# Kernel tuning notes

Hardware: AMD Instinct MI355X
Metric: run time of the kernel (lower is better)

The kernel has to match this reference:

```python
import jax, jax.numpy as jnp
import numpy as np

B, S, H = 2, 2048, 1024
E, K, F = 8, 2, 4096


def setup_inputs() -> dict:
    key = jax.random.key(0)
    ks = jax.random.split(key, 7)
    s_h = 1.0 / np.sqrt(H)
    s_f = 1.0 / np.sqrt(F)
    return {
        "hidden_states": jax.random.normal(ks[0], (B, S, H), jnp.float32),
        "Wr": jax.random.normal(ks[1], (H, E), jnp.float32) * s_h,
        "br": jnp.zeros((E,), jnp.float32),
        "W1": jax.random.normal(ks[2], (E, H, F), jnp.float32) * s_h,
        "b1": jnp.zeros((E, F), jnp.float32),
        "W2": jax.random.normal(ks[3], (E, F, H), jnp.float32) * s_f,
        "b2": jnp.zeros((E, H), jnp.float32),
    }


def _moe_forward(hidden_states, Wr, br, W1, b1, W2, b2):
    b, s, h = hidden_states.shape
    x = hidden_states.reshape(-1, h)  # [T, H]
    # --- router: top-k over softmax probs, renormalized ---
    logits = x @ Wr + br  # [T, E]
    probs = jax.nn.softmax(logits, axis=-1)
    top_w, top_i = jax.lax.top_k(probs, K)  # [T, K]
    weights = top_w / jnp.sum(top_w, axis=-1, keepdims=True)  # [T, K]
    # --- dense-equivalent expert dispatch + combine ---
    # per-token per-expert combine weight (zero for unselected experts)
    out = jnp.zeros_like(x)
    for e in range(E):
        w_e = jnp.sum(weights * (top_i == e), axis=-1)  # [T]
        h_e = jax.nn.gelu(x @ W1[e] + b1[e], approximate=False)  # [T, F]
        y_e = h_e @ W2[e] + b2[e]  # [T, H]
        out = out + w_e[:, None] * y_e
    # --- aux load-balance loss (counts are constants wrt grads) ---
    counts = jnp.sum(jax.nn.one_hot(top_i, E, dtype=logits.dtype), axis=(0, 1))  # [E]
    load = counts / (top_i.size)
    aux_loss = jnp.mean((load - 1.0 / E) ** 2)
    # --- z-loss ---
    z_loss = jnp.mean(jax.nn.logsumexp(logits, axis=-1))
    total_loss = 0.01 * aux_loss + 0.001 * z_loss
    return out.reshape(b, s, h), total_loss


def reference(hidden_states, Wr, br, W1, b1, W2, b2):
    output, total_loss = _moe_forward(hidden_states, Wr, br, W1, b1, W2, b2)
    return output, total_loss
```

## Files before the change

### kernel.cpp

```cpp
#include <hip/hip_runtime.h>
#include <stdint.h>
#include <math.h>

#define T_TOK 4096
#define H_DIM 1024
#define E_EXP 8
#define F_DIM 4096
#define NASSIGN (T_TOK * 2)
#define OUT_ELEMS ((size_t)T_TOK * H_DIM)
#define YB_ELEMS ((size_t)8192 * H_DIM)

typedef unsigned short u16;
typedef __attribute__((ext_vector_type(8))) short short8;
typedef __attribute__((ext_vector_type(4))) short short4v;
typedef __attribute__((ext_vector_type(4))) float f32x4;

__device__ __forceinline__ u16 f2bf(float f) {
  union { float f; uint32_t u; } c; c.f = f;
  uint32_t u = c.u;
  return (u16)((u + 0x7FFFu + ((u >> 16) & 1u)) >> 16);
}

__device__ __forceinline__ float fast_erf(float u) {
  const float au = fabsf(u);
  const float t = __builtin_amdgcn_rcpf(__builtin_fmaf(0.3275911f, au, 1.0f));
  float p = __builtin_fmaf(1.061405429f, t, -1.453152027f);
  p = __builtin_fmaf(p, t, 1.421413741f);
  p = __builtin_fmaf(p, t, -0.284496736f);
  p = __builtin_fmaf(p, t, 0.254829592f);
  p = p * t;
  const float y = __builtin_fmaf(-p, __expf(-au * au), 1.0f);
  return copysignf(y, u);
}

__device__ __forceinline__ void gl_lds16(const void* g, void* l) {
  __builtin_amdgcn_global_load_lds(
      (const __attribute__((address_space(1))) uint32_t*)g,
      (__attribute__((address_space(3))) uint32_t*)(uintptr_t)l, 16, 0, 0);
}


__device__ __forceinline__ void transpose_tile(
    const float* __restrict__ in, u16* __restrict__ out, int R, int C,
    int bx, int by, int bz, u16 (*tile)[72]) {
  const size_t eoff = (size_t)bz * R * C;
  {
    const int c4 = (threadIdx.x & 15) * 4;
    const int rr = threadIdx.x >> 4;
    const float* inp = in + eoff + ((size_t)by * 64) * C + bx * 64;
#pragma unroll
    for (int p = 0; p < 4; ++p) {
      const int r = rr + p * 16;
      const float4 v = *(const float4*)(inp + (size_t)r * C + c4);
      tile[r][c4 + 0] = f2bf(v.x); tile[r][c4 + 1] = f2bf(v.y);
      tile[r][c4 + 2] = f2bf(v.z); tile[r][c4 + 3] = f2bf(v.w);
    }
  }
  __syncthreads();
  {
    u16* op = out + (((size_t)bz * (C >> 6) + bx) * (R >> 6) + by) * 4096;
#pragma unroll
    for (int p = 0; p < 2; ++p) {
      const int c = (threadIdx.x >> 3) + p * 32;
      const int rg = (threadIdx.x & 7) * 8;
      short8 o;
#pragma unroll
      for (int j = 0; j < 8; ++j) o[j] = (short)tile[rg + j][c];
      *(short8*)(op + c * 64 + rg) = o;
    }
  }
}

__global__ __launch_bounds__(256) void prep_kernel(
    const float* __restrict__ x, const float* __restrict__ Wr,
    const float* __restrict__ br, u16* __restrict__ xb,
    int* __restrict__ tki, float* __restrict__ tkw,
    int* __restrict__ counts, float* __restrict__ zsum,
    const float* __restrict__ W1, u16* __restrict__ w1t,
    const float* __restrict__ W2, u16* __restrict__ w2t) {
  __shared__ u16 tile[64][72];
  __shared__ int lcnt[8];
  __shared__ float lzv[16];
  const int id = blockIdx.x;

  if (id >= 256) {
    if (id < 8448) {
      const int q = id - 256;
      transpose_tile(W1, w1t, H_DIM, F_DIM, q & 63, (q >> 6) & 15, q >> 10, tile);
    } else {
      const int q = id - 8448;
      transpose_tile(W2, w2t, F_DIM, H_DIM, q & 15, (q >> 4) & 63, q >> 10, tile);
    }
    return;
  }

  const int wave = threadIdx.x >> 6;
  const int lane = threadIdx.x & 63;
  if (threadIdx.x < 8) lcnt[threadIdx.x] = 0;
  __syncthreads();
#pragma unroll
  for (int it = 0; it < 4; ++it) {
    const int t = id * 16 + wave * 4 + it;
    const float* xr = x + (size_t)t * H_DIM;
    u16* xbr = xb + (size_t)t * H_DIM;
    float acc[8];
#pragma unroll
    for (int e = 0; e < 8; ++e) acc[e] = 0.0f;
#pragma unroll
    for (int j = 0; j < 4; ++j) {
      const int h0 = j * 256 + lane * 4;
      const float4 xv = *(const float4*)(xr + h0);
      const float vv[4] = {xv.x, xv.y, xv.z, xv.w};
      short4v pk;
#pragma unroll
      for (int i = 0; i < 4; ++i) {
        pk[i] = (short)f2bf(vv[i]);
        const float4 w0 = *(const float4*)(Wr + (size_t)(h0 + i) * 8);
        const float4 w1 = *(const float4*)(Wr + (size_t)(h0 + i) * 8 + 4);
        acc[0] += vv[i] * w0.x; acc[1] += vv[i] * w0.y;
        acc[2] += vv[i] * w0.z; acc[3] += vv[i] * w0.w;
        acc[4] += vv[i] * w1.x; acc[5] += vv[i] * w1.y;
        acc[6] += vv[i] * w1.z; acc[7] += vv[i] * w1.w;
      }
      *(short4v*)(xbr + h0) = pk;
    }
#pragma unroll
    for (int e = 0; e < 8; ++e) {
      float v = acc[e];
#pragma unroll
      for (int s = 32; s > 0; s >>= 1) v += __shfl_xor(v, s);
      acc[e] = v;
    }
    if (lane == 0) {
      float l[8];
#pragma unroll
      for (int e = 0; e < 8; ++e) l[e] = acc[e] + br[e];
      float mx = l[0];
#pragma unroll
      for (int e = 1; e < 8; ++e) mx = fmaxf(mx, l[e]);
      float p[8], s = 0.0f;
#pragma unroll
      for (int e = 0; e < 8; ++e) { p[e] = __expf(l[e] - mx); s += p[e]; }
      int i0 = 0;
#pragma unroll
      for (int e = 1; e < 8; ++e) if (p[e] > p[i0]) i0 = e;
      int i1 = (i0 == 0) ? 1 : 0;
#pragma unroll
      for (int e = 0; e < 8; ++e) if (e != i1 && e != i0 && p[e] > p[i1]) i1 = e;
      const float ws = p[i0] + p[i1];
      tki[2 * t] = i0; tki[2 * t + 1] = i1;
      tkw[2 * t] = p[i0] / ws; tkw[2 * t + 1] = p[i1] / ws;
      atomicAdd(&lcnt[i0], 1);
      atomicAdd(&lcnt[i1], 1);
      lzv[wave * 4 + it] = mx + logf(s);
    }
  }
  __syncthreads();
  if (threadIdx.x < 8) {
    const int c = lcnt[threadIdx.x];
    if (c) atomicAdd(&counts[threadIdx.x], c);
  }
  if (threadIdx.x == 64) {
    float zs = 0.0f;
#pragma unroll
    for (int i = 0; i < 16; ++i) zs += lzv[i];
    atomicAdd(zsum, zs);
  }
}

__global__ void scatter_kernel(const int* __restrict__ tki, const float* __restrict__ tkw,
                               const int* __restrict__ counts, int* __restrict__ cursor,
                               int* __restrict__ perm, float* __restrict__ pw,
                               int* __restrict__ islot,
                               const float* __restrict__ zsum, float* __restrict__ out_loss) {
  int offs[8];
  {
    int a = 0;
#pragma unroll
    for (int e = 0; e < 8; ++e) { offs[e] = a; a += counts[e]; }
  }
  const int lane = threadIdx.x & 63;
  const int t = blockIdx.x * 256 + threadIdx.x;
#pragma unroll
  for (int k = 0; k < 2; ++k) {
    const int e = tki[2 * t + k];
    int slot = 0;
#pragma unroll
    for (int ee = 0; ee < 8; ++ee) {
      const unsigned long long mask = __ballot(e == ee);
      if (mask) {
        const int leader = __ffsll(mask) - 1;
        int b = 0;
        if (lane == leader) b = atomicAdd(&cursor[ee], (int)__popcll(mask));
        b = __shfl(b, leader);
        if (e == ee) {
          const int r = (int)__popcll(mask & ((1ull << lane) - 1ull));
          slot = offs[ee] + b + r;
        }
      }
    }
    perm[slot] = t;
    pw[slot] = tkw[2 * t + k];
    islot[2 * t + k] = slot;
  }
  if (blockIdx.x == 0 && threadIdx.x == 0) {
    float aux = 0.0f;
#pragma unroll
    for (int e = 0; e < 8; ++e) {
      const float d = (float)counts[e] / (float)NASSIGN - 0.125f;
      aux += d * d;
    }
    aux *= (1.0f / 8.0f);
    out_loss[0] = 0.01f * aux + 0.001f * (zsum[0] / (float)T_TOK);
  }
}


__global__ __launch_bounds__(256, 4) void gemm1_kernel(
    const u16* __restrict__ xb, const u16* __restrict__ w1t,
    const float* __restrict__ b1, const int* __restrict__ perm,
    const int* __restrict__ cnts, u16* __restrict__ hbuf) {
  const int id = blockIdx.x;
  const int e = id & 7;
  const int wq = id >> 3;
  const int n0 = (wq & 31) << 7;
  const int m0 = (wq >> 5) << 7;
  int cnt, off;
  {
    int a = 0, c = 0;
#pragma unroll
    for (int i = 0; i < 8; ++i) { const int ci = cnts[i]; if (i < e) a += ci; if (i == e) c = ci; }
    cnt = c; off = a;
  }
  if (m0 >= cnt) return;

  __shared__ __align__(16) u16 smem[16384];
  u16* As = smem;
  u16* Bs = smem + 8192;

  const int tid = threadIdx.x;
  const int rbase = tid >> 3;
  const int kc = ((tid & 7) ^ (rbase & 7)) * 8;

  const u16* ap[4];
#pragma unroll
  for (int l = 0; l < 4; ++l) {
    int ra = m0 + rbase + l * 32; if (ra > cnt - 1) ra = cnt - 1;
    ap[l] = xb + (size_t)perm[off + ra] * H_DIM + kc;
  }
  const u16* bp0 = w1t + ((((size_t)e * (F_DIM >> 6) + (n0 >> 6)) * (H_DIM >> 6)) << 12)
                 + rbase * 64 + kc;
  const size_t bnt = (size_t)(H_DIM >> 6) << 12;

  const int wave = tid >> 6, lane = tid & 63;
  const int wm = (wave >> 1) * 64, wn = (wave & 1) * 64;
  const int lr = lane & 15, q = lane >> 4;
  const int qs0 = q ^ (lr & 7), qs1 = (4 + q) ^ (lr & 7);

  f32x4 acc[4][4];
#pragma unroll
  for (int i = 0; i < 4; ++i)
#pragma unroll
    for (int j = 0; j < 4; ++j) acc[i][j] = (f32x4)0.0f;

  const short8* Afr = (const short8*)As;
  const short8* Bfr = (const short8*)Bs;

  for (int k0 = 0; k0 < (H_DIM >> 6); ++k0) {
    gl_lds16(ap[0], &As[(size_t)tid * 8]);
    gl_lds16(ap[1], &As[(size_t)(tid + 256) * 8]);
    gl_lds16(ap[2], &As[(size_t)(tid + 512) * 8]);
    gl_lds16(ap[3], &As[(size_t)(tid + 768) * 8]);
    gl_lds16(bp0,              &Bs[(size_t)tid * 8]);
    gl_lds16(bp0 + 2048,       &Bs[(size_t)(tid + 256) * 8]);
    gl_lds16(bp0 + bnt,        &Bs[(size_t)(tid + 512) * 8]);
    gl_lds16(bp0 + bnt + 2048, &Bs[(size_t)(tid + 768) * 8]);
#pragma unroll
    for (int l = 0; l < 4; ++l) ap[l] += 64;
    bp0 += 4096;
    __syncthreads();
#pragma unroll
    for (int s = 0; s < 2; ++s) {
      const int qs = s ? qs1 : qs0;
      short8 a[4], b[4];
#pragma unroll
      for (int i = 0; i < 4; ++i) a[i] = Afr[(wm + i * 16 + lr) * 8 + qs];
#pragma unroll
      for (int j = 0; j < 4; ++j) b[j] = Bfr[(wn + j * 16 + lr) * 8 + qs];
#pragma unroll
      for (int i = 0; i < 4; ++i)
#pragma unroll
        for (int j = 0; j < 4; ++j)
          acc[i][j] = __builtin_amdgcn_mfma_f32_16x16x32_bf16(a[i], b[j], acc[i][j], 0, 0, 0);
    }
    __syncthreads();
  }

#pragma unroll
  for (int i = 0; i < 4; ++i) {
#pragma unroll
    for (int rr = 0; rr < 4; ++rr) {
      const int row = wm + i * 16 + q * 4 + rr;
#pragma unroll
      for (int j = 0; j < 4; ++j) {
        const int col = wn + j * 16 + lr;
        const float v = acc[i][j][rr] + b1[e * F_DIM + n0 + col];
        const float g = 0.5f * v * (1.0f + fast_erf(v * 0.70710678118654752f));
        smem[(row << 7) + (col ^ (q << 4))] = f2bf(g);
      }
    }
  }
  __syncthreads();
#pragma unroll
  for (int p = 0; p < 8; ++p) {
    const int ml = p * 16 + (tid >> 4);
    const int nl = (tid & 15) * 8;
    const int m = m0 + ml;
    if (m < cnt) {
      const int qq = (ml >> 2) & 3;
      *(short8*)(hbuf + (size_t)(off + m) * F_DIM + n0 + nl) =
          *(const short8*)(smem + (ml << 7) + (nl ^ (qq << 4)));
    }
  }
}

__global__ __launch_bounds__(256, 4) void gemm2_kernel(
    const u16* __restrict__ hbuf, const u16* __restrict__ w2t,
    const float* __restrict__ b2, const float* __restrict__ pw,
    const int* __restrict__ cnts, float* __restrict__ ybuf) {
  const int id = blockIdx.x;
  const int e = id & 7;
  const int wq = id >> 3;
  const int n0 = (wq & 7) << 7;
  const int ks = (wq >> 3) & 1;
  const int m0 = (wq >> 4) << 7;
  int cnt, off;
  {
    int a = 0, c = 0;
#pragma unroll
    for (int i = 0; i < 8; ++i) { const int ci = cnts[i]; if (i < e) a += ci; if (i == e) c = ci; }
    cnt = c; off = a;
  }
  if (m0 >= cnt) return;

  __shared__ __align__(16) u16 As[128 * 64];
  __shared__ __align__(16) u16 Bs[128 * 64];

  const int tid = threadIdx.x;
  const int rbase = tid >> 3;
  const int kc = ((tid & 7) ^ (rbase & 7)) * 8;

  const u16* ap[4];
#pragma unroll
  for (int l = 0; l < 4; ++l) {
    int ra = m0 + rbase + l * 32; if (ra > cnt - 1) ra = cnt - 1;
    ap[l] = hbuf + (size_t)(off + ra) * F_DIM + (ks << 11) + kc;
  }
  const u16* bp0 = w2t + ((((size_t)e * (H_DIM >> 6) + (n0 >> 6)) * (F_DIM >> 6)) << 12)
                 + ((size_t)(ks << 5) << 12) + rbase * 64 + kc;
  const size_t bnt = (size_t)(F_DIM >> 6) << 12;

  const int wave = tid >> 6, lane = tid & 63;
  const int wm = (wave >> 1) * 64, wn = (wave & 1) * 64;
  const int lr = lane & 15, q = lane >> 4;
  const int qs0 = q ^ (lr & 7), qs1 = (4 + q) ^ (lr & 7);

  f32x4 acc[4][4];
#pragma unroll
  for (int i = 0; i < 4; ++i)
#pragma unroll
    for (int j = 0; j < 4; ++j) acc[i][j] = (f32x4)0.0f;

  const short8* Afr = (const short8*)As;
  const short8* Bfr = (const short8*)Bs;

  for (int k0 = 0; k0 < 32; ++k0) {
    gl_lds16(ap[0], &As[(size_t)tid * 8]);
    gl_lds16(ap[1], &As[(size_t)(tid + 256) * 8]);
    gl_lds16(ap[2], &As[(size_t)(tid + 512) * 8]);
    gl_lds16(ap[3], &As[(size_t)(tid + 768) * 8]);
    gl_lds16(bp0,              &Bs[(size_t)tid * 8]);
    gl_lds16(bp0 + 2048,       &Bs[(size_t)(tid + 256) * 8]);
    gl_lds16(bp0 + bnt,        &Bs[(size_t)(tid + 512) * 8]);
    gl_lds16(bp0 + bnt + 2048, &Bs[(size_t)(tid + 768) * 8]);
#pragma unroll
    for (int l = 0; l < 4; ++l) ap[l] += 64;
    bp0 += 4096;
    __syncthreads();
#pragma unroll
    for (int s = 0; s < 2; ++s) {
      const int qs = s ? qs1 : qs0;
      short8 a[4], b[4];
#pragma unroll
      for (int i = 0; i < 4; ++i) a[i] = Afr[(wm + i * 16 + lr) * 8 + qs];
#pragma unroll
      for (int j = 0; j < 4; ++j) b[j] = Bfr[(wn + j * 16 + lr) * 8 + qs];
#pragma unroll
      for (int i = 0; i < 4; ++i)
#pragma unroll
        for (int j = 0; j < 4; ++j)
          acc[i][j] = __builtin_amdgcn_mfma_f32_16x16x32_bf16(a[i], b[j], acc[i][j], 0, 0, 0);
    }
    __syncthreads();
  }

  float* yb = ybuf + (size_t)ks * YB_ELEMS;
#pragma unroll
  for (int i = 0; i < 4; ++i) {
#pragma unroll
    for (int rr = 0; rr < 4; ++rr) {
      const int m = m0 + wm + i * 16 + q * 4 + rr;
      if (m < cnt) {
        const int slot = off + m;
        const float w = pw[slot];
        float* orow = yb + (size_t)slot * H_DIM;
#pragma unroll
        for (int j = 0; j < 4; ++j) {
          const int col = n0 + wn + j * 16 + lr;
          float y = acc[i][j][rr];
          if (ks == 0) y += b2[e * H_DIM + col];
          orow[col] = w * y;
        }
      }
    }
  }
}

__global__ __launch_bounds__(256) void combine_kernel(
    const float* __restrict__ ybuf, const int* __restrict__ islot,
    float* __restrict__ out) {
  const int t = blockIdx.x;
  const int s0 = islot[2 * t];
  const int s1 = islot[2 * t + 1];
  const int c = threadIdx.x * 4;
  const float4 a0 = *(const float4*)(ybuf + (size_t)s0 * H_DIM + c);
  const float4 a1 = *(const float4*)(ybuf + YB_ELEMS + (size_t)s0 * H_DIM + c);
  const float4 b0 = *(const float4*)(ybuf + (size_t)s1 * H_DIM + c);
  const float4 b1 = *(const float4*)(ybuf + YB_ELEMS + (size_t)s1 * H_DIM + c);
  float4 r;
  r.x = a0.x + a1.x + b0.x + b1.x;
  r.y = a0.y + a1.y + b0.y + b1.y;
  r.z = a0.z + a1.z + b0.z + b1.z;
  r.w = a0.w + a1.w + b0.w + b1.w;
  *(float4*)(out + (size_t)t * H_DIM + c) = r;
}


extern "C" void kernel_launch(void* const* d_in, const int* in_sizes, int n_in,
                              void* d_out, int out_size, void* d_ws, size_t ws_size,
                              hipStream_t stream) {
  const float* x  = (const float*)d_in[0];
  const float* Wr = (const float*)d_in[1];
  const float* br = (const float*)d_in[2];
  const float* W1 = (const float*)d_in[3];
  const float* b1 = (const float*)d_in[4];
  const float* W2 = (const float*)d_in[5];
  const float* b2 = (const float*)d_in[6];
  float* out = (float*)d_out;

  char* ws = (char*)d_ws;
  u16* xb    = (u16*)(ws);
  u16* w1t   = (u16*)(ws + 8388608ull);
  u16* w2t   = (u16*)(ws + 75497472ull);
  u16* hbuf  = (u16*)(ws + 142606336ull);
  float* ybuf = (float*)(ws + 8388608ull);
  int*   tki    = (int*)(ws + 209715200ull);
  float* tkw    = (float*)(ws + 209747968ull);
  int*   perm   = (int*)(ws + 209780736ull);
  float* pw     = (float*)(ws + 209813504ull);
  int*   counts = (int*)(ws + 209846272ull);
  int*   cursor = counts + 8;
  float* zsum   = (float*)(counts + 16);
  int*   islot  = (int*)(ws + 209846400ull);

  hipMemsetAsync(counts, 0, 128, stream);

  prep_kernel<<<16640, 256, 0, stream>>>(x, Wr, br, xb, tki, tkw, counts, zsum,
                                         W1, w1t, W2, w2t);
  scatter_kernel<<<T_TOK / 256, 256, 0, stream>>>(tki, tkw, counts, cursor, perm, pw,
                                                  islot, zsum, out + OUT_ELEMS);
  gemm1_kernel<<<8192, 256, 0, stream>>>(xb, w1t, b1, perm, counts, hbuf);
  gemm2_kernel<<<4096, 256, 0, stream>>>(hbuf, w2t, b2, pw, counts, ybuf);
  combine_kernel<<<T_TOK, 256, 0, stream>>>(ybuf, islot, out);
}
```

Baseline: 608.9 us.

## Enlarge expert GEMM tiles to 256x256 with double-buffered LDS staging

Both expert GEMM kernels move from 128x128 to 256x256 output tiles per workgroup, with each wave computing a 128x128 sub-tile from an 8x8 accumulator array. LDS is double-buffered (two 64 KB stages) and the next K-slice is issued before computing the current one, with an explicit vmcnt wait and raw barriers. The aim is more reuse per loaded byte and overlap of global loads with MFMA work. In exchange, occupancy drops to one workgroup per CU with heavy register pressure, and there are fewer blocks to cover ragged per-expert token counts. The transpose tile padding also changes from 72 to 73.

```diff
diff --git a/kernel.cpp b/kernel.cpp
--- a/kernel.cpp
+++ b/kernel.cpp
@@ -39,10 +39,15 @@
       (__attribute__((address_space(3))) uint32_t*)(uintptr_t)l, 16, 0, 0);
 }
 
+__device__ __forceinline__ void wg_barrier() {
+  asm volatile("" ::: "memory");
+  __builtin_amdgcn_s_barrier();
+  asm volatile("" ::: "memory");
+}
 
 __device__ __forceinline__ void transpose_tile(
     const float* __restrict__ in, u16* __restrict__ out, int R, int C,
-    int bx, int by, int bz, u16 (*tile)[72]) {
+    int bx, int by, int bz, u16 (*tile)[73]) {
   const size_t eoff = (size_t)bz * R * C;
   {
     const int c4 = (threadIdx.x & 15) * 4;
@@ -78,7 +83,7 @@
     int* __restrict__ counts, float* __restrict__ zsum,
     const float* __restrict__ W1, u16* __restrict__ w1t,
     const float* __restrict__ W2, u16* __restrict__ w2t) {
-  __shared__ u16 tile[64][72];
+  __shared__ u16 tile[64][73];
   __shared__ int lcnt[8];
   __shared__ float lzv[16];
   const int id = blockIdx.x;
@@ -216,15 +221,45 @@
 }
 
 
-__global__ __launch_bounds__(256, 4) void gemm1_kernel(
+#define STAGE16(BUFOFF)                                                  \
+  {                                                                      \
+    const int nb_ = (BUFOFF);                                            \
+    _Pragma("unroll")                                                    \
+    for (int l = 0; l < 8; ++l) {                                        \
+      gl_lds16(ap[l], &smem[nb_ + l * 2048 + tid * 8]);          ap[l] += 64; \
+      gl_lds16(bp[l], &smem[nb_ + 16384 + l * 2048 + tid * 8]);  bp[l] += 4096; \
+    }                                                                    \
+  }
+
+#define COMPUTE256(BUFOFF)                                               \
+  {                                                                      \
+    const short8* Af = (const short8*)(smem + (BUFOFF));                 \
+    const short8* Bf = Af + 2048;                                        \
+    _Pragma("unroll")                                                    \
+    for (int s = 0; s < 2; ++s) {                                        \
+      const int qs = s ? qs1 : qs0;                                      \
+      short8 a[8];                                                       \
+      _Pragma("unroll")                                                  \
+      for (int i = 0; i < 8; ++i) a[i] = Af[(wm + i * 16 + lr) * 8 + qs]; \
+      _Pragma("unroll")                                                  \
+      for (int j = 0; j < 8; ++j) {                                      \
+        const short8 b = Bf[(wn + j * 16 + lr) * 8 + qs];                \
+        _Pragma("unroll")                                                \
+        for (int i = 0; i < 8; ++i)                                      \
+          acc[i][j] = __builtin_amdgcn_mfma_f32_16x16x32_bf16(a[i], b, acc[i][j], 0, 0, 0); \
+      }                                                                  \
+    }                                                                    \
+  }
+
+__global__ __launch_bounds__(256, 1) void gemm1_kernel(
     const u16* __restrict__ xb, const u16* __restrict__ w1t,
     const float* __restrict__ b1, const int* __restrict__ perm,
     const int* __restrict__ cnts, u16* __restrict__ hbuf) {
   const int id = blockIdx.x;
   const int e = id & 7;
   const int wq = id >> 3;
-  const int n0 = (wq & 31) << 7;
-  const int m0 = (wq >> 5) << 7;
+  const int n0 = (wq & 15) << 8;
+  const int m0 = (wq >> 4) << 8;
   int cnt, off;
   {
     int a = 0, c = 0;
@@ -234,106 +269,90 @@
   }
   if (m0 >= cnt) return;
 
-  __shared__ __align__(16) u16 smem[16384];
-  u16* As = smem;
-  u16* Bs = smem + 8192;
+  __shared__ __align__(16) u16 smem[65536];
 
   const int tid = threadIdx.x;
   const int rbase = tid >> 3;
   const int kc = ((tid & 7) ^ (rbase & 7)) * 8;
 
-  const u16* ap[4];
-#pragma unroll
-  for (int l = 0; l < 4; ++l) {
+  const u16* ap[8];
+#pragma unroll
+  for (int l = 0; l < 8; ++l) {
     int ra = m0 + rbase + l * 32; if (ra > cnt - 1) ra = cnt - 1;
     ap[l] = xb + (size_t)perm[off + ra] * H_DIM + kc;
   }
-  const u16* bp0 = w1t + ((((size_t)e * (F_DIM >> 6) + (n0 >> 6)) * (H_DIM >> 6)) << 12)
-                 + rbase * 64 + kc;
-  const size_t bnt = (size_t)(H_DIM >> 6) << 12;
+  const u16* bp[8];
+#pragma unroll
+  for (int l = 0; l < 8; ++l)
+    bp[l] = w1t + (((size_t)e * (F_DIM >> 6) + (n0 >> 6) + (l >> 1)) * (H_DIM >> 6)) * 4096
+          + ((l & 1) * 32 + rbase) * 64 + kc;
 
   const int wave = tid >> 6, lane = tid & 63;
-  const int wm = (wave >> 1) * 64, wn = (wave & 1) * 64;
+  const int wm = (wave >> 1) * 128, wn = (wave & 1) * 128;
   const int lr = lane & 15, q = lane >> 4;
   const int qs0 = q ^ (lr & 7), qs1 = (4 + q) ^ (lr & 7);
 
-  f32x4 acc[4][4];
-#pragma unroll
-  for (int i = 0; i < 4; ++i)
-#pragma unroll
-    for (int j = 0; j < 4; ++j) acc[i][j] = (f32x4)0.0f;
-
-  const short8* Afr = (const short8*)As;
-  const short8* Bfr = (const short8*)Bs;
-
-  for (int k0 = 0; k0 < (H_DIM >> 6); ++k0) {
-    gl_lds16(ap[0], &As[(size_t)tid * 8]);
-    gl_lds16(ap[1], &As[(size_t)(tid + 256) * 8]);
-    gl_lds16(ap[2], &As[(size_t)(tid + 512) * 8]);
-    gl_lds16(ap[3], &As[(size_t)(tid + 768) * 8]);
-    gl_lds16(bp0,              &Bs[(size_t)tid * 8]);
-    gl_lds16(bp0 + 2048,       &Bs[(size_t)(tid + 256) * 8]);
-    gl_lds16(bp0 + bnt,        &Bs[(size_t)(tid + 512) * 8]);
-    gl_lds16(bp0 + bnt + 2048, &Bs[(size_t)(tid + 768) * 8]);
-#pragma unroll
-    for (int l = 0; l < 4; ++l) ap[l] += 64;
-    bp0 += 4096;
-    __syncthreads();
-#pragma unroll
-    for (int s = 0; s < 2; ++s) {
-      const int qs = s ? qs1 : qs0;
-      short8 a[4], b[4];
-#pragma unroll
-      for (int i = 0; i < 4; ++i) a[i] = Afr[(wm + i * 16 + lr) * 8 + qs];
-#pragma unroll
-      for (int j = 0; j < 4; ++j) b[j] = Bfr[(wn + j * 16 + lr) * 8 + qs];
-#pragma unroll
-      for (int i = 0; i < 4; ++i)
-#pragma unroll
-        for (int j = 0; j < 4; ++j)
-          acc[i][j] = __builtin_amdgcn_mfma_f32_16x16x32_bf16(a[i], b[j], acc[i][j], 0, 0, 0);
-    }
-    __syncthreads();
-  }
-
-#pragma unroll
-  for (int i = 0; i < 4; ++i) {
+  f32x4 acc[8][8];
+#pragma unroll
+  for (int i = 0; i < 8; ++i)
+#pragma unroll
+    for (int j = 0; j < 8; ++j) acc[i][j] = (f32x4)0.0f;
+
+  int cur = 0;
+  STAGE16(0);
+  for (int k0 = 0; k0 < (H_DIM >> 6) - 1; ++k0) {
+    STAGE16((cur ^ 1) << 15);
+    asm volatile("s_waitcnt vmcnt(16)" ::: "memory");
+    __builtin_amdgcn_sched_barrier(0);
+    wg_barrier();
+    COMPUTE256(cur << 15);
+    wg_barrier();
+    cur ^= 1;
+  }
+  asm volatile("s_waitcnt vmcnt(0)" ::: "memory");
+  __builtin_amdgcn_sched_barrier(0);
+  wg_barrier();
+  COMPUTE256(cur << 15);
+  wg_barrier();
+
+#pragma unroll
+  for (int i = 0; i < 8; ++i) {
 #pragma unroll
     for (int rr = 0; rr < 4; ++rr) {
       const int row = wm + i * 16 + q * 4 + rr;
 #pragma unroll
-      for (int j = 0; j < 4; ++j) {
+      for (int j = 0; j < 8; ++j) {
         const int col = wn + j * 16 + lr;
         const float v = acc[i][j][rr] + b1[e * F_DIM + n0 + col];
         const float g = 0.5f * v * (1.0f + fast_erf(v * 0.70710678118654752f));
-        smem[(row << 7) + (col ^ (q << 4))] = f2bf(g);
+        smem[(row << 8) + (col ^ (q << 4))] = f2bf(g);
       }
     }
   }
   __syncthreads();
 #pragma unroll
-  for (int p = 0; p < 8; ++p) {
-    const int ml = p * 16 + (tid >> 4);
-    const int nl = (tid & 15) * 8;
-    const int m = m0 + ml;
+  for (int p = 0; p < 32; ++p) {
+    const int row = p * 8 + (tid >> 5);
+    const int c8 = (tid & 31) * 8;
+    const int m = m0 + row;
     if (m < cnt) {
-      const int qq = (ml >> 2) & 3;
-      *(short8*)(hbuf + (size_t)(off + m) * F_DIM + n0 + nl) =
-          *(const short8*)(smem + (ml << 7) + (nl ^ (qq << 4)));
-    }
-  }
-}
-
-__global__ __launch_bounds__(256, 4) void gemm2_kernel(
+      const int qq = (row >> 2) & 3;
+      *(short8*)(hbuf + (size_t)(off + m) * F_DIM + n0 + c8) =
+          *(const short8*)(smem + (row << 8) + (c8 ^ (qq << 4)));
+    }
+  }
+}
+
+__global__ __launch_bounds__(256, 1) void gemm2_kernel(
     const u16* __restrict__ hbuf, const u16* __restrict__ w2t,
     const float* __restrict__ b2, const float* __restrict__ pw,
     const int* __restrict__ cnts, float* __restrict__ ybuf) {
   const int id = blockIdx.x;
   const int e = id & 7;
   const int wq = id >> 3;
-  const int n0 = (wq & 7) << 7;
-  const int ks = (wq >> 3) & 1;
-  const int m0 = (wq >> 4) << 7;
+  const int n0 = (wq & 3) << 8;
+  const int ks = (wq >> 2) & 1;
+  const int m0 = (wq >> 3) << 8;
   int cnt, off;
   {
     int a = 0, c = 0;
@@ -343,70 +362,54 @@
   }
   if (m0 >= cnt) return;
 
-  __shared__ __align__(16) u16 As[128 * 64];
-  __shared__ __align__(16) u16 Bs[128 * 64];
+  __shared__ __align__(16) u16 smem[65536];
 
   const int tid = threadIdx.x;
   const int rbase = tid >> 3;
   const int kc = ((tid & 7) ^ (rbase & 7)) * 8;
 
-  const u16* ap[4];
-#pragma unroll
-  for (int l = 0; l < 4; ++l) {
+  const u16* ap[8];
+#pragma unroll
+  for (int l = 0; l < 8; ++l) {
     int ra = m0 + rbase + l * 32; if (ra > cnt - 1) ra = cnt - 1;
     ap[l] = hbuf + (size_t)(off + ra) * F_DIM + (ks << 11) + kc;
   }
-  const u16* bp0 = w2t + ((((size_t)e * (H_DIM >> 6) + (n0 >> 6)) * (F_DIM >> 6)) << 12)
-                 + ((size_t)(ks << 5) << 12) + rbase * 64 + kc;
-  const size_t bnt = (size_t)(F_DIM >> 6) << 12;
+  const u16* bp[8];
+#pragma unroll
+  for (int l = 0; l < 8; ++l)
+    bp[l] = w2t + (((size_t)e * (H_DIM >> 6) + (n0 >> 6) + (l >> 1)) * (F_DIM >> 6)
+                   + (ks << 5)) * 4096 + ((l & 1) * 32 + rbase) * 64 + kc;
 
   const int wave = tid >> 6, lane = tid & 63;
-  const int wm = (wave >> 1) * 64, wn = (wave & 1) * 64;
+  const int wm = (wave >> 1) * 128, wn = (wave & 1) * 128;
   const int lr = lane & 15, q = lane >> 4;
   const int qs0 = q ^ (lr & 7), qs1 = (4 + q) ^ (lr & 7);
 
-  f32x4 acc[4][4];
-#pragma unroll
-  for (int i = 0; i < 4; ++i)
-#pragma unroll
-    for (int j = 0; j < 4; ++j) acc[i][j] = (f32x4)0.0f;
-
-  const short8* Afr = (const short8*)As;
-  const short8* Bfr = (const short8*)Bs;
-
-  for (int k0 = 0; k0 < 32; ++k0) {
-    gl_lds16(ap[0], &As[(size_t)tid * 8]);
-    gl_lds16(ap[1], &As[(size_t)(tid + 256) * 8]);
-    gl_lds16(ap[2], &As[(size_t)(tid + 512) * 8]);
-    gl_lds16(ap[3], &As[(size_t)(tid + 768) * 8]);
-    gl_lds16(bp0,              &Bs[(size_t)tid * 8]);
-    gl_lds16(bp0 + 2048,       &Bs[(size_t)(tid + 256) * 8]);
-    gl_lds16(bp0 + bnt,        &Bs[(size_t)(tid + 512) * 8]);
-    gl_lds16(bp0 + bnt + 2048, &Bs[(size_t)(tid + 768) * 8]);
-#pragma unroll
-    for (int l = 0; l < 4; ++l) ap[l] += 64;
-    bp0 += 4096;
-    __syncthreads();
-#pragma unroll
-    for (int s = 0; s < 2; ++s) {
-      const int qs = s ? qs1 : qs0;
-      short8 a[4], b[4];
-#pragma unroll
-      for (int i = 0; i < 4; ++i) a[i] = Afr[(wm + i * 16 + lr) * 8 + qs];
-#pragma unroll
-      for (int j = 0; j < 4; ++j) b[j] = Bfr[(wn + j * 16 + lr) * 8 + qs];
-#pragma unroll
-      for (int i = 0; i < 4; ++i)
-#pragma unroll
-        for (int j = 0; j < 4; ++j)
-          acc[i][j] = __builtin_amdgcn_mfma_f32_16x16x32_bf16(a[i], b[j], acc[i][j], 0, 0, 0);
-    }
-    __syncthreads();
-  }
+  f32x4 acc[8][8];
+#pragma unroll
+  for (int i = 0; i < 8; ++i)
+#pragma unroll
+    for (int j = 0; j < 8; ++j) acc[i][j] = (f32x4)0.0f;
+
+  int cur = 0;
+  STAGE16(0);
+  for (int k0 = 0; k0 < 31; ++k0) {
+    STAGE16((cur ^ 1) << 15);
+    asm volatile("s_waitcnt vmcnt(16)" ::: "memory");
+    __builtin_amdgcn_sched_barrier(0);
+    wg_barrier();
+    COMPUTE256(cur << 15);
+    wg_barrier();
+    cur ^= 1;
+  }
+  asm volatile("s_waitcnt vmcnt(0)" ::: "memory");
+  __builtin_amdgcn_sched_barrier(0);
+  wg_barrier();
+  COMPUTE256(cur << 15);
 
   float* yb = ybuf + (size_t)ks * YB_ELEMS;
 #pragma unroll
-  for (int i = 0; i < 4; ++i) {
+  for (int i = 0; i < 8; ++i) {
 #pragma unroll
     for (int rr = 0; rr < 4; ++rr) {
       const int m = m0 + wm + i * 16 + q * 4 + rr;
@@ -415,7 +418,7 @@
         const float w = pw[slot];
         float* orow = yb + (size_t)slot * H_DIM;
 #pragma unroll
-        for (int j = 0; j < 4; ++j) {
+        for (int j = 0; j < 8; ++j) {
           const int col = n0 + wn + j * 16 + lr;
           float y = acc[i][j][rr];
           if (ks == 0) y += b2[e * H_DIM + col];
@@ -479,7 +482,7 @@
                                          W1, w1t, W2, w2t);
   scatter_kernel<<<T_TOK / 256, 256, 0, stream>>>(tki, tkw, counts, cursor, perm, pw,
                                                   islot, zsum, out + OUT_ELEMS);
-  gemm1_kernel<<<8192, 256, 0, stream>>>(xb, w1t, b1, perm, counts, hbuf);
-  gemm2_kernel<<<4096, 256, 0, stream>>>(hbuf, w2t, b2, pw, counts, ybuf);
+  gemm1_kernel<<<2048, 256, 0, stream>>>(xb, w1t, b1, perm, counts, hbuf);
+  gemm2_kernel<<<1024, 256, 0, stream>>>(hbuf, w2t, b2, pw, counts, ybuf);
   combine_kernel<<<T_TOK, 256, 0, stream>>>(ybuf, islot, out);
 }
```

After: 760.1 us. +24.8%, slower.
